# Optimization experiments

Hardware: AMD Instinct MI355X
Metric: run time of the kernel (lower is better)

The kernel has to match this reference:

```python
import jax, jax.numpy as jnp
import numpy as np

N = 65536; NPG = 4096; D_IN = 34; EMB = 34; S_DIM = 4; P_DIM = 22
WIDTH = 126; NUM_CLASSES = 8; K = 8; NUM_CONVS = 2


def setup_inputs() -> dict:
    key = jax.random.key(0)
    ks = iter(jax.random.split(key, 64))

    def w(shape, fan_in):
        return jax.random.normal(next(ks), shape, dtype=jnp.float32) / np.float32(np.sqrt(fan_in))

    inp = {
        "x": jax.random.normal(next(ks), (N, D_IN), dtype=jnp.float32),
        "conv_Ws": w((NUM_CONVS, EMB, S_DIM), EMB),
        "conv_bs": jnp.zeros((NUM_CONVS, S_DIM), jnp.float32),
        "conv_Wh": w((NUM_CONVS, EMB, P_DIM), EMB),
        "conv_bh": jnp.zeros((NUM_CONVS, P_DIM), jnp.float32),
        "conv_Wo": w((NUM_CONVS, EMB + 2 * P_DIM, EMB), EMB + 2 * P_DIM),
        "conv_bo": jnp.zeros((NUM_CONVS, EMB), jnp.float32),
    }
    for name, out_dim in (("id", NUM_CLASSES), ("reg", 4), ("chg", 1)):
        inp[name + "_W0"] = w((EMB, WIDTH), EMB)
        inp[name + "_b0"] = jnp.zeros((WIDTH,), jnp.float32)
        inp[name + "_Wh"] = w((2, WIDTH, WIDTH), WIDTH)
        inp[name + "_bh"] = jnp.zeros((2, WIDTH), jnp.float32)
        inp[name + "_Wf"] = w((WIDTH, out_dim), WIDTH)
        inp[name + "_bf"] = jnp.zeros((out_dim,), jnp.float32)
    inp["n_per_graph"] = NPG
    return inp


def _mlp(x, W0, b0, Wh, bh, Wf, bf):
    h = jax.nn.elu(x @ W0 + b0)
    h = jax.nn.elu(h @ Wh[0] + bh[0])
    h = jax.nn.elu(h @ Wh[1] + bh[1])
    return h @ Wf + bf


def _gravnet(xg, Ws, bs, Wh, bh, Wo, bo, k):
    # xg: [G, n, EMB]; equal-sized graphs (PyG batch with equal event sizes)
    s = xg @ Ws + bs  # [G, n, S_DIM] learned space coords
    h = xg @ Wh + bh  # [G, n, P_DIM] propagated features

    def per_graph(s1, h1):
        # full pairwise sq-distances in learned space (self included, d=0)
        d2 = jnp.sum((s1[:, None, :] - s1[None, :, :]) ** 2, axis=-1)  # [n, n]
        _, idx = jax.lax.top_k(-jax.lax.stop_gradient(d2), k)  # [n, k]
        s_nb = s1[idx]  # [n, k, S_DIM]
        d2k = jnp.sum((s1[:, None, :] - s_nb) ** 2, axis=-1)  # [n, k]
        w = jnp.exp(-10.0 * d2k)  # GravNet edge weight
        msg = h1[idx] * w[..., None]  # [n, k, P_DIM]
        return jnp.mean(msg, axis=1), jnp.max(msg, axis=1)

    mean_agg, max_agg = jax.vmap(per_graph)(s, h)  # [G, n, P_DIM] each
    out = jnp.concatenate([xg, mean_agg, max_agg], axis=-1) @ Wo + bo
    return out


def reference(x, conv_Ws, conv_bs, conv_Wh, conv_bh, conv_Wo, conv_bo,
              id_W0, id_b0, id_Wh, id_bh, id_Wf, id_bf,
              reg_W0, reg_b0, reg_Wh, reg_bh, reg_Wf, reg_bf,
              chg_W0, chg_b0, chg_Wh, chg_bh, chg_Wf, chg_bf,
              n_per_graph):
    n = int(n_per_graph)
    G = x.shape[0] // n
    emb = x.reshape(G, n, -1)  # native_mlpf=False: embedding = input
    for i in range(NUM_CONVS):
        emb = _gravnet(emb, conv_Ws[i], conv_bs[i], conv_Wh[i], conv_bh[i],
                       conv_Wo[i], conv_bo[i], K)
    emb = emb.reshape(x.shape[0], -1)
    preds_id = _mlp(emb, id_W0, id_b0, id_Wh, id_bh, id_Wf, id_bf)
    preds_momentum = _mlp(emb, reg_W0, reg_b0, reg_Wh, reg_bh, reg_Wf, reg_bf) + x[:, 1:5]
    pred_charge = _mlp(emb, chg_W0, chg_b0, chg_Wh, chg_bh, chg_Wf, chg_bf)
    return preds_id, preds_momentum, pred_charge
```

## Files before the change

kernel.cpp:

```cpp
#include <hip/hip_runtime.h>
#include <math.h>

#define N_NODES 65536
#define NPG     4096
#define D_IN    34
#define EMB     34
#define S_DIM   4
#define P_DIM   22
#define CONCAT  78
#define WIDTH   126
#define KNN     8
#define HPAD    24
#define EPAD    36
#define TILE    1024
#define NSPLIT  16
#define FBIG    3.4e38f
#define ASTR    133
#define WFSTR   9
#define TRUNCM  0xFFFFF000u

__device__ __forceinline__ float elu1(float v) {
    return v > 0.f ? v : expm1f(v);
}

__device__ __forceinline__ bool lexlt(float da, int ja, float db, int jb) {
    return (da < db) || (da == db && ja < jb);
}


__device__ __forceinline__ void ins4u(unsigned (&k)[4], unsigned key) {
    unsigned c = min(key, k[0]);
#pragma unroll
    for (int r = 3; r >= 1; --r) {
        const unsigned hi = max(k[r], c);
        k[r] = min(k[r], c);
        c = hi;
    }
    k[0] = c;
}

__device__ __forceinline__ void clean8u(unsigned (&k)[8]) {
#define CASU(i, j2) { const unsigned hi = max(k[i], k[j2]); \
    const unsigned lo = min(k[i], k[j2]); k[i] = hi; k[j2] = lo; }
    CASU(0,4) CASU(1,5) CASU(2,6) CASU(3,7)
    CASU(0,2) CASU(1,3) CASU(4,6) CASU(5,7)
    CASU(0,1) CASU(2,3) CASU(4,5) CASU(6,7)
#undef CASU
}

__device__ __forceinline__ void merge8u(unsigned (&k)[8], int m) {
    unsigned p[8];
#pragma unroll
    for (int i = 0; i < 8; ++i) p[i] = (unsigned)__shfl_xor((int)k[i], m);
#pragma unroll
    for (int i = 0; i < 8; ++i) k[i] = min(k[i], p[7 - i]);
    clean8u(k);
}

__device__ __forceinline__ void ins8(float (&d)[8], int (&ix)[8], float dd, int jj) {
    const bool s0 = dd < d[0];
    d[0] = s0 ? dd : d[0]; ix[0] = s0 ? jj : ix[0];
#pragma unroll
    for (int r = 0; r < 7; ++r) {
        const bool s = d[r] < d[r + 1];
        const float a = s ? d[r + 1] : d[r], b = s ? d[r] : d[r + 1];
        const int   x = s ? ix[r + 1] : ix[r], y = s ? ix[r] : ix[r + 1];
        d[r] = a; d[r + 1] = b; ix[r] = x; ix[r + 1] = y;
    }
}

__device__ __forceinline__ void clean8(float (&md)[8], int (&mj)[8]) {
#define CASL(i, k) { const bool sw = lexlt(md[i], mj[i], md[k], mj[k]); \
    const float a = sw ? md[k] : md[i], b = sw ? md[i] : md[k]; \
    const int   x = sw ? mj[k] : mj[i], y = sw ? mj[i] : mj[k]; \
    md[i] = a; md[k] = b; mj[i] = x; mj[k] = y; }
    CASL(0,4) CASL(1,5) CASL(2,6) CASL(3,7)
    CASL(0,2) CASL(1,3) CASL(4,6) CASL(5,7)
    CASL(0,1) CASL(2,3) CASL(4,5) CASL(6,7)
#undef CASL
}

__device__ __forceinline__ void merge8(float (&md)[8], int (&mj)[8], int m) {
    float pd[8]; int pj[8];
#pragma unroll
    for (int i = 0; i < 8; ++i) { pd[i] = __shfl_xor(md[i], m); pj[i] = __shfl_xor(mj[i], m); }
#pragma unroll
    for (int i = 0; i < 8; ++i) {
        const bool lt = lexlt(md[i], mj[i], pd[7 - i], pj[7 - i]);
        const float nd = lt ? md[i] : pd[7 - i];
        const int   nj = lt ? mj[i] : pj[7 - i];
        md[i] = nd; mj[i] = nj;
    }
    clean8(md, mj);
}

__global__ __launch_bounds__(256) void sh_kernel(
        const float* __restrict__ emb, int eld,
        const float* __restrict__ Ws, const float* __restrict__ bs,
        const float* __restrict__ Wh, const float* __restrict__ bh,
        float* __restrict__ s_out, float* __restrict__ h_out,
        int* __restrict__ fcnt) {
    if (blockIdx.x == 0 && threadIdx.x == 0) fcnt[0] = 0;

    __shared__ float lWs[EMB * S_DIM];
    __shared__ float lWh[EMB * P_DIM];
    __shared__ float lbs[S_DIM];
    __shared__ float lbh[P_DIM];
    for (int t = threadIdx.x; t < EMB * S_DIM; t += 256) lWs[t] = Ws[t];
    for (int t = threadIdx.x; t < EMB * P_DIM; t += 256) lWh[t] = Wh[t];
    if (threadIdx.x < S_DIM) lbs[threadIdx.x] = bs[threadIdx.x];
    if (threadIdx.x < P_DIM) lbh[threadIdx.x] = bh[threadIdx.x];
    __syncthreads();

    const int n = blockIdx.x * 256 + threadIdx.x;
    const float* __restrict__ row = emb + (size_t)n * eld;
    float e[EMB];
#pragma unroll
    for (int r = 0; r < EMB; ++r) e[r] = row[r];

    float s[S_DIM], h[P_DIM];
#pragma unroll
    for (int c = 0; c < S_DIM; ++c) s[c] = lbs[c];
#pragma unroll
    for (int c = 0; c < P_DIM; ++c) h[c] = lbh[c];
#pragma unroll
    for (int r = 0; r < EMB; ++r) {
        const float er = e[r];
#pragma unroll
        for (int c = 0; c < S_DIM; ++c) s[c] = fmaf(er, lWs[r * S_DIM + c], s[c]);
#pragma unroll
        for (int c = 0; c < P_DIM; ++c) h[c] = fmaf(er, lWh[r * P_DIM + c], h[c]);
    }
    ((float4*)s_out)[n] = make_float4(s[0], s[1], s[2], s[3]);
    float* __restrict__ hr = h_out + (size_t)n * HPAD;
#pragma unroll
    for (int c = 0; c < P_DIM; ++c) hr[c] = h[c];
}

__global__ __launch_bounds__(256, 4) void grav_scan(
        const float* __restrict__ s_buf,
        int* __restrict__ knnj,
        int* __restrict__ fcnt, int* __restrict__ flist) {
    __shared__ float4 sl[TILE];

    const int g     = blockIdx.x >> 7;
    const int chunk = blockIdx.x & 127;
    const int gbase = g * NPG;
    const int tid   = threadIdx.x;
    const int ql    = tid & 15;
    const int grp   = tid >> 4;
    const int nA    = gbase + chunk * 32 + grp * 2;
    const int nB    = nA + 1;

    const float4* __restrict__ sg = (const float4*)s_buf + gbase;
    float4 pre[4];
#pragma unroll
    for (int i = 0; i < 4; ++i) pre[i] = sg[tid + 256 * i];
    const float4 siA = ((const float4*)s_buf)[nA];
    const float4 siB = ((const float4*)s_buf)[nB];

    unsigned kA[4], kB[4];
#pragma unroll
    for (int r = 0; r < 4; ++r) { kA[r] = 0xFFFFFFFFu; kB[r] = 0xFFFFFFFFu; }

#pragma unroll
    for (int i = 0; i < 4; ++i) sl[tid + 256 * i] = pre[i];
    __syncthreads();

    for (int t = 0; t < NPG / TILE; ++t) {
        if (t < NPG / TILE - 1) {
#pragma unroll
            for (int i = 0; i < 4; ++i)
                pre[i] = sg[(t + 1) * TILE + tid + 256 * i];
        }
        unsigned suff = ((unsigned)(t << 10)) | (unsigned)ql;
#pragma unroll 4
        for (int s = 0; s < TILE / NSPLIT; ++s) {
            const float4 sj = sl[NSPLIT * s + ql];
            {
                const float dx = siA.x - sj.x, dy = siA.y - sj.y;
                const float dz = siA.z - sj.z, dw = siA.w - sj.w;
                const float d2 = fmaf(dx, dx, fmaf(dy, dy, fmaf(dz, dz, dw * dw)));
                ins4u(kA, (__float_as_uint(d2) & TRUNCM) | suff);
            }
            {
                const float dx = siB.x - sj.x, dy = siB.y - sj.y;
                const float dz = siB.z - sj.z, dw = siB.w - sj.w;
                const float d2 = fmaf(dx, dx, fmaf(dy, dy, fmaf(dz, dz, dw * dw)));
                ins4u(kB, (__float_as_uint(d2) & TRUNCM) | suff);
            }
            suff += 16u;
        }
        if (t < NPG / TILE - 1) {
            __syncthreads();
#pragma unroll
            for (int i = 0; i < 4; ++i) sl[tid + 256 * i] = pre[i];
            __syncthreads();
        }
    }

    {
        unsigned md[8];
        md[0] = kA[0]; md[1] = kA[1]; md[2] = kA[2]; md[3] = kA[3];
        md[4] = (unsigned)__shfl_xor((int)kA[3], 1);
        md[5] = (unsigned)__shfl_xor((int)kA[2], 1);
        md[6] = (unsigned)__shfl_xor((int)kA[1], 1);
        md[7] = (unsigned)__shfl_xor((int)kA[0], 1);
        clean8u(md);
        merge8u(md, 2);
        merge8u(md, 4);
        merge8u(md, 8);

        const unsigned truncW = md[0] & TRUNCM;
        int ci = 0;
#pragma unroll
        for (int r = 0; r < 4; ++r) ci += ((kA[r] & TRUNCM) <= truncW) ? 1 : 0;
        int v = ci + ((ci == 4) ? 256 : 0);
#pragma unroll
        for (int m = 1; m <= 8; m <<= 1) v += __shfl_xor(v, m);
        const bool flag = ((v & 0xFF) > 8) || ((v >> 8) != 0);

        unsigned ks = md[0];
#pragma unroll
        for (int r = 1; r < 8; ++r) { const bool p = (ql == r); ks = p ? md[r] : ks; }
        if (ql < 8)
            knnj[(size_t)nA * 8 + ql] = (int)(((ks >> 4) & 0xFFu) * 16u + (ks & 0xFu));
        if (ql == 0 && flag) {
            const int slot = atomicAdd(fcnt, 1);
            flist[slot] = nA;
        }
    }

    {
        unsigned md[8];
        md[0] = kB[0]; md[1] = kB[1]; md[2] = kB[2]; md[3] = kB[3];
        md[4] = (unsigned)__shfl_xor((int)kB[3], 1);
        md[5] = (unsigned)__shfl_xor((int)kB[2], 1);
        md[6] = (unsigned)__shfl_xor((int)kB[1], 1);
        md[7] = (unsigned)__shfl_xor((int)kB[0], 1);
        clean8u(md);
        merge8u(md, 2);
        merge8u(md, 4);
        merge8u(md, 8);

        const unsigned truncW = md[0] & TRUNCM;
        int ci = 0;
#pragma unroll
        for (int r = 0; r < 4; ++r) ci += ((kB[r] & TRUNCM) <= truncW) ? 1 : 0;
        int v = ci + ((ci == 4) ? 256 : 0);
#pragma unroll
        for (int m = 1; m <= 8; m <<= 1) v += __shfl_xor(v, m);
        const bool flag = ((v & 0xFF) > 8) || ((v >> 8) != 0);

        unsigned ks = md[0];
#pragma unroll
        for (int r = 1; r < 8; ++r) { const bool p = (ql == r); ks = p ? md[r] : ks; }
        if (ql < 8)
            knnj[(size_t)nB * 8 + ql] = (int)(((ks >> 4) & 0xFFu) * 16u + (ks & 0xFu));
        if (ql == 0 && flag) {
            const int slot = atomicAdd(fcnt, 1);
            flist[slot] = nB;
        }
    }
}

__global__ __launch_bounds__(256, 4) void grav_fix(
        const float* __restrict__ s_buf,
        int* __restrict__ knnj,
        const int* __restrict__ fcnt, const int* __restrict__ flist) {
    const int cnt = fcnt[0];
    const int ql  = threadIdx.x & 15;
    const int ngroups = gridDim.x * 16;

    for (int idx = blockIdx.x * 16 + (threadIdx.x >> 4); idx < cnt; idx += ngroups) {
        const int node = flist[idx];
        const int gbase = node & ~(NPG - 1);
        const float4 si = ((const float4*)s_buf)[node];
        const float4* __restrict__ sg = (const float4*)s_buf + gbase;

        float fd[8]; int fj[8];
#pragma unroll
        for (int r = 0; r < 8; ++r) { fd[r] = FBIG; fj[r] = 0; }
#pragma unroll 4
        for (int k = 0; k < NPG / NSPLIT; ++k) {
            const int j = NSPLIT * k + ql;
            const float4 sj = sg[j];
            const float dx = si.x - sj.x, dy = si.y - sj.y;
            const float dz = si.z - sj.z, dw = si.w - sj.w;
            const float d2 = fmaf(dx, dx, fmaf(dy, dy, fmaf(dz, dz, dw * dw)));
            ins8(fd, fj, d2, j);
        }
        merge8(fd, fj, 1);
        merge8(fd, fj, 2);
        merge8(fd, fj, 4);
        merge8(fd, fj, 8);

        int js = fj[0];
#pragma unroll
        for (int r = 1; r < 8; ++r) { const bool p = (ql == r); js = p ? fj[r] : js; }
        if (ql < 8) knnj[(size_t)node * 8 + ql] = js;
    }
}

template <int ELD, bool TOUT>
__global__ __launch_bounds__(256, 4) void grav_gather(
        const float* __restrict__ emb_in,
        const float* __restrict__ s_buf,
        const float* __restrict__ h_buf,
        const int* __restrict__ knnj,
        const float* __restrict__ Wo, const float* __restrict__ bo,
        float* __restrict__ out) {
    __shared__ float wot[EMB * 81];
    __shared__ float bol[EMB];
    __shared__ float cc[64][49];

    const int tid = threadIdx.x;
    const int q   = tid & 3;
    const int nl  = tid >> 2;
    const int node = blockIdx.x * 64 + nl;
    const int gbase = node & ~(NPG - 1);

    for (int t = tid; t < CONCAT * EMB; t += 256) {
        const int r = t / EMB, c = t % EMB;
        wot[c * 81 + r] = Wo[t];
    }
    if (tid < EMB) bol[tid] = bo[tid];

    const float4 si = ((const float4*)s_buf)[node];
    const int ja = knnj[(size_t)node * 8 + q];
    const int jb = knnj[(size_t)node * 8 + 4 + q];
    const float4 sja = ((const float4*)s_buf)[gbase + ja];
    const float4 sjb = ((const float4*)s_buf)[gbase + jb];
    float wa, wb;
    {
        const float dx = si.x - sja.x, dy = si.y - sja.y;
        const float dz = si.z - sja.z, dw = si.w - sja.w;
        wa = expf(-10.f * fmaf(dx, dx, fmaf(dy, dy, fmaf(dz, dz, dw * dw))));
    }
    {
        const float dx = si.x - sjb.x, dy = si.y - sjb.y;
        const float dz = si.z - sjb.z, dw = si.w - sjb.w;
        wb = expf(-10.f * fmaf(dx, dx, fmaf(dy, dy, fmaf(dz, dz, dw * dw))));
    }
    const float4* __restrict__ ha = (const float4*)(h_buf + (size_t)(gbase + ja) * HPAD);
    const float4* __restrict__ hb = (const float4*)(h_buf + (size_t)(gbase + jb) * HPAD);

#pragma unroll
    for (int ch = 0; ch < 6; ++ch) {
        const float4 qa = ha[ch], qb = hb[ch];
        float sx = fmaf(wa, qa.x, wb * qb.x), sy = fmaf(wa, qa.y, wb * qb.y);
        float sz = fmaf(wa, qa.z, wb * qb.z), sw = fmaf(wa, qa.w, wb * qb.w);
        float mx = fmaxf(wa * qa.x, wb * qb.x), my = fmaxf(wa * qa.y, wb * qb.y);
        float mz = fmaxf(wa * qa.z, wb * qb.z), mw = fmaxf(wa * qa.w, wb * qb.w);
#pragma unroll
        for (int m = 1; m <= 2; m <<= 1) {
            sx += __shfl_xor(sx, m); sy += __shfl_xor(sy, m);
            sz += __shfl_xor(sz, m); sw += __shfl_xor(sw, m);
            mx = fmaxf(mx, __shfl_xor(mx, m)); my = fmaxf(my, __shfl_xor(my, m));
            mz = fmaxf(mz, __shfl_xor(mz, m)); mw = fmaxf(mw, __shfl_xor(mw, m));
        }
        if (q == (ch & 3)) {
            cc[nl][ch * 4 + 0] = sx * 0.125f; cc[nl][ch * 4 + 1] = sy * 0.125f;
            cc[nl][ch * 4 + 2] = sz * 0.125f; cc[nl][ch * 4 + 3] = sw * 0.125f;
            cc[nl][24 + ch * 4 + 0] = mx; cc[nl][24 + ch * 4 + 1] = my;
            cc[nl][24 + ch * 4 + 2] = mz; cc[nl][24 + ch * 4 + 3] = mw;
        }
    }
    __syncthreads();

    float e[EMB];
    const float* __restrict__ erow = emb_in + (size_t)node * ELD;
    if constexpr (ELD == 34) {
#pragma unroll
        for (int i = 0; i < 17; ++i) {
            const float2 v = ((const float2*)erow)[i];
            e[2 * i] = v.x; e[2 * i + 1] = v.y;
        }
    } else {
#pragma unroll
        for (int i = 0; i < 8; ++i) {
            const float4 v = ((const float4*)erow)[i];
            e[4 * i] = v.x; e[4 * i + 1] = v.y; e[4 * i + 2] = v.z; e[4 * i + 3] = v.w;
        }
        const float2 v = ((const float2*)erow)[16];
        e[32] = v.x; e[33] = v.y;
    }

#pragma unroll
    for (int m = 0; m < 9; ++m) {
        const int c = q + 4 * m;
        if (c < EMB) {
            const float* __restrict__ wr = &wot[c * 81];
            float acc = bol[c];
#pragma unroll
            for (int r = 0; r < EMB; ++r)   acc = fmaf(e[r], wr[r], acc);
#pragma unroll
            for (int p = 0; p < P_DIM; ++p) acc = fmaf(cc[nl][p], wr[34 + p], acc);
#pragma unroll
            for (int p = 0; p < P_DIM; ++p) acc = fmaf(cc[nl][24 + p], wr[56 + p], acc);
            if constexpr (TOUT)
                out[(size_t)c * N_NODES + node] = acc;
            else
                out[(size_t)node * EPAD + c] = acc;
        }
    }
}

__global__ __launch_bounds__(512, 4) void heads_fused(
        const float* __restrict__ emb2T,
        const float* __restrict__ xin,
        float* __restrict__ outp,
        const float* __restrict__ W0a, const float* __restrict__ b0a,
        const float* __restrict__ Wha, const float* __restrict__ bha,
        const float* __restrict__ Wfa, const float* __restrict__ bfa,
        const float* __restrict__ W0b, const float* __restrict__ b0b,
        const float* __restrict__ Whb, const float* __restrict__ bhb,
        const float* __restrict__ Wfb, const float* __restrict__ bfb,
        const float* __restrict__ W0c, const float* __restrict__ b0c,
        const float* __restrict__ Whc, const float* __restrict__ bhc,
        const float* __restrict__ Wfc, const float* __restrict__ bfc) {
    __shared__ float sA[WIDTH * ASTR];
    __shared__ float sWf[128 * WFSTR];

    const int tid  = threadIdx.x;
    const int head = blockIdx.x % 3;
    const int rowbase = (blockIdx.x / 3) * 128;
    const int lane = tid & 63;
    const int wave = __builtin_amdgcn_readfirstlane(tid >> 6);
    int colbase = wave * 16;
    if (colbase > WIDTH - 16) colbase = WIDTH - 16;

    const float* W0 = head == 0 ? W0a : head == 1 ? W0b : W0c;
    const float* b0 = head == 0 ? b0a : head == 1 ? b0b : b0c;
    const float* Wh = head == 0 ? Wha : head == 1 ? Whb : Whc;
    const float* bh = head == 0 ? bha : head == 1 ? bhb : bhc;
    const float* Wf = head == 0 ? Wfa : head == 1 ? Wfb : Wfc;
    const float* bf = head == 0 ? bfa : head == 1 ? bfb : bfc;
    const int odim  = head == 0 ? 8 : head == 1 ? 4 : 1;
    const size_t ooff = head == 0 ? 0
                      : head == 1 ? (size_t)N_NODES * 8 : (size_t)N_NODES * 12;

    for (int t = tid; t < 128 * 8; t += 512) {
        const int k = t >> 3, o = t & 7;
        sWf[k * WFSTR + o] = (k < WIDTH && o < odim) ? Wf[k * odim + o] : 0.f;
    }

    float accA[16], accB[16];

#pragma unroll
    for (int o = 0; o < 16; ++o) { accA[o] = b0[colbase + o]; accB[o] = accA[o]; }
#pragma unroll 2
    for (int k = 0; k < EMB; ++k) {
        const float xa = emb2T[(size_t)k * N_NODES + rowbase + lane];
        const float xb = emb2T[(size_t)k * N_NODES + rowbase + lane + 64];
        const float* __restrict__ wr = W0 + (size_t)k * WIDTH + colbase;
#pragma unroll
        for (int o = 0; o < 16; ++o) {
            const float w = wr[o];
            accA[o] = fmaf(xa, w, accA[o]);
            accB[o] = fmaf(xb, w, accB[o]);
        }
    }
    __syncthreads();
#pragma unroll
    for (int o = 0; o < 16; ++o) {
        sA[(colbase + o) * ASTR + lane]      = elu1(accA[o]);
        sA[(colbase + o) * ASTR + lane + 64] = elu1(accB[o]);
    }
    __syncthreads();

#pragma unroll
    for (int o = 0; o < 16; ++o) { accA[o] = bh[colbase + o]; accB[o] = accA[o]; }
#pragma unroll 2
    for (int k = 0; k < WIDTH; ++k) {
        const float xa = sA[k * ASTR + lane];
        const float xb = sA[k * ASTR + lane + 64];
        const float* __restrict__ wr = Wh + (size_t)k * WIDTH + colbase;
#pragma unroll
        for (int o = 0; o < 16; ++o) {
            const float w = wr[o];
            accA[o] = fmaf(xa, w, accA[o]);
            accB[o] = fmaf(xb, w, accB[o]);
        }
    }
    __syncthreads();
#pragma unroll
    for (int o = 0; o < 16; ++o) {
        sA[(colbase + o) * ASTR + lane]      = elu1(accA[o]);
        sA[(colbase + o) * ASTR + lane + 64] = elu1(accB[o]);
    }
    __syncthreads();

#pragma unroll
    for (int o = 0; o < 16; ++o) { accA[o] = bh[WIDTH + colbase + o]; accB[o] = accA[o]; }
#pragma unroll 2
    for (int k = 0; k < WIDTH; ++k) {
        const float xa = sA[k * ASTR + lane];
        const float xb = sA[k * ASTR + lane + 64];
        const float* __restrict__ wr = Wh + (size_t)(WIDTH + k) * WIDTH + colbase;
#pragma unroll
        for (int o = 0; o < 16; ++o) {
            const float w = wr[o];
            accA[o] = fmaf(xa, w, accA[o]);
            accB[o] = fmaf(xb, w, accB[o]);
        }
    }
    __syncthreads();
#pragma unroll
    for (int o = 0; o < 16; ++o) {
        sA[(colbase + o) * ASTR + lane]      = elu1(accA[o]);
        sA[(colbase + o) * ASTR + lane + 64] = elu1(accB[o]);
    }
    __syncthreads();

#pragma unroll 2
    for (int r = 0; r < 16; ++r) {
        const int rowl = wave * 16 + r;
        const float xa0 = sA[lane * ASTR + rowl];
        const float xa1 = (lane + 64 < WIDTH) ? sA[(lane + 64) * ASTR + rowl] : 0.f;
        float pa[8];
#pragma unroll
        for (int o = 0; o < 8; ++o) {
            const float w0 = sWf[lane * WFSTR + o];
            const float w1 = sWf[(lane + 64) * WFSTR + o];
            pa[o] = fmaf(xa0, w0, xa1 * w1);
        }
#pragma unroll
        for (int m = 1; m <= 32; m <<= 1) {
#pragma unroll
            for (int o = 0; o < 8; ++o) pa[o] += __shfl_xor(pa[o], m);
        }
        if (lane < odim) {
            float v = pa[0];
#pragma unroll
            for (int o = 1; o < 8; ++o) { const bool p = (lane == o); v = p ? pa[o] : v; }
            v += bf[lane];
            const int grow = rowbase + rowl;
            if (head == 1) v += xin[(size_t)grow * D_IN + 1 + lane];
            outp[ooff + (size_t)grow * odim + lane] = v;
        }
    }
}

extern "C" void kernel_launch(void* const* d_in, const int* in_sizes, int n_in,
                              void* d_out, int out_size, void* d_ws, size_t ws_size,
                              hipStream_t stream) {
    (void)in_sizes; (void)n_in; (void)out_size;

    const float* x   = (const float*)d_in[0];
    const float* cWs = (const float*)d_in[1];
    const float* cbs = (const float*)d_in[2];
    const float* cWh = (const float*)d_in[3];
    const float* cbh = (const float*)d_in[4];
    const float* cWo = (const float*)d_in[5];
    const float* cbo = (const float*)d_in[6];
    const float* hW0[3] = {(const float*)d_in[7],  (const float*)d_in[13], (const float*)d_in[19]};
    const float* hb0[3] = {(const float*)d_in[8],  (const float*)d_in[14], (const float*)d_in[20]};
    const float* hWh[3] = {(const float*)d_in[9],  (const float*)d_in[15], (const float*)d_in[21]};
    const float* hbh[3] = {(const float*)d_in[10], (const float*)d_in[16], (const float*)d_in[22]};
    const float* hWf[3] = {(const float*)d_in[11], (const float*)d_in[17], (const float*)d_in[23]};
    const float* hbf[3] = {(const float*)d_in[12], (const float*)d_in[18], (const float*)d_in[24]};
    float* outp = (float*)d_out;
    float* ws = (float*)d_ws;

    const size_t OFF_S   = 0;
    const size_t OFF_H   = OFF_S   + (size_t)N_NODES * 4;
    const size_t OFF_E1  = OFF_H   + (size_t)N_NODES * HPAD;
    const size_t OFF_E2T = OFF_E1  + (size_t)N_NODES * EPAD;
    const size_t OFF_KS  = OFF_E2T + (size_t)EMB * N_NODES;
    const size_t WS_END  = OFF_KS  + (size_t)N_NODES * 10;
    if (ws_size < WS_END * sizeof(float)) return;

    float* s_buf  = ws + OFF_S;
    float* h_buf  = ws + OFF_H;
    float* emb1   = ws + OFF_E1;
    float* emb2T  = ws + OFF_E2T;
    int*   knnj   = (int*)(ws + OFF_KS);
    int*   flist  = (int*)(ws + OFF_KS + (size_t)N_NODES * 8);
    int*   fcnt   = (int*)(ws + OFF_KS + (size_t)N_NODES * 9);

    sh_kernel<<<256, 256, 0, stream>>>(x, D_IN, cWs, cbs, cWh, cbh, s_buf, h_buf, fcnt);
    grav_scan<<<2048, 256, 0, stream>>>(s_buf, knnj, fcnt, flist);
    grav_fix<<<256, 256, 0, stream>>>(s_buf, knnj, fcnt, flist);
    grav_gather<34, false><<<1024, 256, 0, stream>>>(x, s_buf, h_buf, knnj, cWo, cbo, emb1);

    sh_kernel<<<256, 256, 0, stream>>>(emb1, EPAD, cWs + EMB * S_DIM, cbs + S_DIM,
                                       cWh + EMB * P_DIM, cbh + P_DIM, s_buf, h_buf, fcnt);
    grav_scan<<<2048, 256, 0, stream>>>(s_buf, knnj, fcnt, flist);
    grav_fix<<<256, 256, 0, stream>>>(s_buf, knnj, fcnt, flist);
    grav_gather<36, true><<<1024, 256, 0, stream>>>(emb1, s_buf, h_buf, knnj,
                                                    cWo + CONCAT * EMB, cbo + EMB, emb2T);

    heads_fused<<<1536, 512, 0, stream>>>(
        emb2T, x, outp,
        hW0[0], hb0[0], hWh[0], hbh[0], hWf[0], hbf[0],
        hW0[1], hb0[1], hWh[1], hbh[1], hWf[1], hbf[1],
        hW0[2], hb0[2], hWh[2], hbh[2], hWf[2], hbf[2]);
}
```

Before: 776.0 us.

## Run MLP heads on bf16 MFMA with split hi/lo precision emulation

Replaces the scalar-FMA MLP heads kernel with one that uses 16x16x32 bf16 MFMA instructions. Activations and weights are each split into bf16 hi and lo parts, and three MFMAs per tile recover close to fp32 accuracy. A new prep kernel packs the head weights into the fragment layout each call. Each block now handles 64 rows, with activations kept in LDS as bf16 hi/lo. The aim is to move the dominant GEMM work from vector ALUs onto matrix cores, at the cost of three times the MFMA count and a small amount of precision loss.

```diff
diff --git a/kernel.cpp b/kernel.cpp
--- a/kernel.cpp
+++ b/kernel.cpp
@@ -15,9 +15,14 @@
 #define TILE    1024
 #define NSPLIT  16
 #define FBIG    3.4e38f
-#define ASTR    133
-#define WFSTR   9
 #define TRUNCM  0xFFFFF000u
+
+#define KSTR    136
+#define WSEG0   0
+#define WSEG1   8192
+#define WSEG2   24576
+#define WSEG3   40960
+#define WHEAD   43008
 
 __device__ __forceinline__ float elu1(float v) {
     return v > 0.f ? v : expm1f(v);
@@ -27,6 +32,13 @@
     return (da < db) || (da == db && ja < jb);
 }
 
+__device__ __forceinline__ unsigned short f2bf(float v) {
+    const unsigned u = __float_as_uint(v);
+    return (unsigned short)((u + 0x7FFFu + ((u >> 16) & 1u)) >> 16);
+}
+__device__ __forceinline__ float bf2f(unsigned short h) {
+    return __uint_as_float(((unsigned)h) << 16);
+}
 
 __device__ __forceinline__ void ins4u(unsigned (&k)[4], unsigned key) {
     unsigned c = min(key, k[0]);
@@ -406,138 +418,185 @@
     }
 }
 
-__global__ __launch_bounds__(512, 4) void heads_fused(
+__global__ __launch_bounds__(256) void prep_wfrag(
+        const float* __restrict__ W0a, const float* __restrict__ Wha, const float* __restrict__ Wfa,
+        const float* __restrict__ W0b, const float* __restrict__ Whb, const float* __restrict__ Wfb,
+        const float* __restrict__ W0c, const float* __restrict__ Whc, const float* __restrict__ Wfc,
+        unsigned short* __restrict__ whi, unsigned short* __restrict__ wlo) {
+    const int head = blockIdx.y;
+    const int e = blockIdx.x * 256 + threadIdx.x;
+
+    const float* W0 = head == 0 ? W0a : head == 1 ? W0b : W0c;
+    const float* Wh = head == 0 ? Wha : head == 1 ? Whb : Whc;
+    const float* Wf = head == 0 ? Wfa : head == 1 ? Wfb : Wfc;
+    const int odim  = head == 0 ? 8 : head == 1 ? 4 : 1;
+
+    int k, n, K, N, NT, ld, segbase;
+    const float* src;
+    if (e < WSEG1) {
+        const int e2 = e;      k = e2 >> 7; n = e2 & 127;
+        K = EMB; N = WIDTH; NT = 8; ld = WIDTH; src = W0; segbase = WSEG0;
+    } else if (e < WSEG2) {
+        const int e2 = e - WSEG1; k = e2 >> 7; n = e2 & 127;
+        K = WIDTH; N = WIDTH; NT = 8; ld = WIDTH; src = Wh; segbase = WSEG1;
+    } else if (e < WSEG3) {
+        const int e2 = e - WSEG2; k = e2 >> 7; n = e2 & 127;
+        K = WIDTH; N = WIDTH; NT = 8; ld = WIDTH; src = Wh + WIDTH * WIDTH; segbase = WSEG2;
+    } else {
+        const int e2 = e - WSEG3; k = e2 >> 4; n = e2 & 15;
+        K = WIDTH; N = odim; NT = 1; ld = odim; src = Wf; segbase = WSEG3;
+    }
+
+    const float val = (k < K && n < N) ? src[k * ld + n] : 0.f;
+    const unsigned short h = f2bf(val);
+    const unsigned short l = f2bf(val - bf2f(h));
+
+    const int ks = k >> 5, ko = k & 31, nt = n >> 4;
+    const int pos = (((ks * NT + nt) * 64) + ((ko >> 3) * 16) + (n & 15)) * 8 + (ko & 7);
+    whi[(size_t)head * WHEAD + segbase + pos] = h;
+    wlo[(size_t)head * WHEAD + segbase + pos] = l;
+}
+
+typedef __attribute__((ext_vector_type(8))) short bf8;
+typedef __attribute__((ext_vector_type(4))) float f32x4;
+
+__global__ __launch_bounds__(256, 3) void heads_mfma(
         const float* __restrict__ emb2T,
         const float* __restrict__ xin,
         float* __restrict__ outp,
-        const float* __restrict__ W0a, const float* __restrict__ b0a,
-        const float* __restrict__ Wha, const float* __restrict__ bha,
-        const float* __restrict__ Wfa, const float* __restrict__ bfa,
-        const float* __restrict__ W0b, const float* __restrict__ b0b,
-        const float* __restrict__ Whb, const float* __restrict__ bhb,
-        const float* __restrict__ Wfb, const float* __restrict__ bfb,
-        const float* __restrict__ W0c, const float* __restrict__ b0c,
-        const float* __restrict__ Whc, const float* __restrict__ bhc,
-        const float* __restrict__ Wfc, const float* __restrict__ bfc) {
-    __shared__ float sA[WIDTH * ASTR];
-    __shared__ float sWf[128 * WFSTR];
+        const unsigned short* __restrict__ whi,
+        const unsigned short* __restrict__ wlo,
+        const float* __restrict__ b0a, const float* __restrict__ bha, const float* __restrict__ bfa,
+        const float* __restrict__ b0b, const float* __restrict__ bhb, const float* __restrict__ bfb,
+        const float* __restrict__ b0c, const float* __restrict__ bhc, const float* __restrict__ bfc) {
+    __shared__ unsigned short aH[64 * KSTR];
+    __shared__ unsigned short aL[64 * KSTR];
+    __shared__ float pf[4 * 64 * 16];
 
     const int tid  = threadIdx.x;
     const int head = blockIdx.x % 3;
-    const int rowbase = (blockIdx.x / 3) * 128;
-    const int lane = tid & 63;
-    const int wave = __builtin_amdgcn_readfirstlane(tid >> 6);
-    int colbase = wave * 16;
-    if (colbase > WIDTH - 16) colbase = WIDTH - 16;
-
-    const float* W0 = head == 0 ? W0a : head == 1 ? W0b : W0c;
+    const int rowbase = (blockIdx.x / 3) * 64;
+    const int w = tid >> 6;
+    const int l = tid & 63;
+
+    const unsigned short* WH = whi + (size_t)head * WHEAD;
+    const unsigned short* WL = wlo + (size_t)head * WHEAD;
     const float* b0 = head == 0 ? b0a : head == 1 ? b0b : b0c;
-    const float* Wh = head == 0 ? Wha : head == 1 ? Whb : Whc;
     const float* bh = head == 0 ? bha : head == 1 ? bhb : bhc;
-    const float* Wf = head == 0 ? Wfa : head == 1 ? Wfb : Wfc;
     const float* bf = head == 0 ? bfa : head == 1 ? bfb : bfc;
     const int odim  = head == 0 ? 8 : head == 1 ? 4 : 1;
     const size_t ooff = head == 0 ? 0
                       : head == 1 ? (size_t)N_NODES * 8 : (size_t)N_NODES * 12;
 
-    for (int t = tid; t < 128 * 8; t += 512) {
-        const int k = t >> 3, o = t & 7;
-        sWf[k * WFSTR + o] = (k < WIDTH && o < odim) ? Wf[k * odim + o] : 0.f;
-    }
-
-    float accA[16], accB[16];
-
-#pragma unroll
-    for (int o = 0; o < 16; ++o) { accA[o] = b0[colbase + o]; accB[o] = accA[o]; }
-#pragma unroll 2
-    for (int k = 0; k < EMB; ++k) {
-        const float xa = emb2T[(size_t)k * N_NODES + rowbase + lane];
-        const float xb = emb2T[(size_t)k * N_NODES + rowbase + lane + 64];
-        const float* __restrict__ wr = W0 + (size_t)k * WIDTH + colbase;
-#pragma unroll
-        for (int o = 0; o < 16; ++o) {
-            const float w = wr[o];
-            accA[o] = fmaf(xa, w, accA[o]);
-            accB[o] = fmaf(xb, w, accB[o]);
-        }
+    for (int t = tid; t < 64 * 64; t += 256) {
+        const int r = t & 63, k = t >> 6;
+        const float v = (k < EMB) ? emb2T[(size_t)k * N_NODES + rowbase + r] : 0.f;
+        const unsigned short h = f2bf(v);
+        aH[r * KSTR + k] = h;
+        aL[r * KSTR + k] = f2bf(v - bf2f(h));
     }
     __syncthreads();
-#pragma unroll
-    for (int o = 0; o < 16; ++o) {
-        sA[(colbase + o) * ASTR + lane]      = elu1(accA[o]);
-        sA[(colbase + o) * ASTR + lane + 64] = elu1(accB[o]);
-    }
-    __syncthreads();
-
-#pragma unroll
-    for (int o = 0; o < 16; ++o) { accA[o] = bh[colbase + o]; accB[o] = accA[o]; }
-#pragma unroll 2
-    for (int k = 0; k < WIDTH; ++k) {
-        const float xa = sA[k * ASTR + lane];
-        const float xb = sA[k * ASTR + lane + 64];
-        const float* __restrict__ wr = Wh + (size_t)k * WIDTH + colbase;
-#pragma unroll
-        for (int o = 0; o < 16; ++o) {
-            const float w = wr[o];
-            accA[o] = fmaf(xa, w, accA[o]);
-            accB[o] = fmaf(xb, w, accB[o]);
-        }
-    }
-    __syncthreads();
-#pragma unroll
-    for (int o = 0; o < 16; ++o) {
-        sA[(colbase + o) * ASTR + lane]      = elu1(accA[o]);
-        sA[(colbase + o) * ASTR + lane + 64] = elu1(accB[o]);
-    }
-    __syncthreads();
-
-#pragma unroll
-    for (int o = 0; o < 16; ++o) { accA[o] = bh[WIDTH + colbase + o]; accB[o] = accA[o]; }
-#pragma unroll 2
-    for (int k = 0; k < WIDTH; ++k) {
-        const float xa = sA[k * ASTR + lane];
-        const float xb = sA[k * ASTR + lane + 64];
-        const float* __restrict__ wr = Wh + (size_t)(WIDTH + k) * WIDTH + colbase;
-#pragma unroll
-        for (int o = 0; o < 16; ++o) {
-            const float w = wr[o];
-            accA[o] = fmaf(xa, w, accA[o]);
-            accB[o] = fmaf(xb, w, accB[o]);
-        }
-    }
-    __syncthreads();
-#pragma unroll
-    for (int o = 0; o < 16; ++o) {
-        sA[(colbase + o) * ASTR + lane]      = elu1(accA[o]);
-        sA[(colbase + o) * ASTR + lane + 64] = elu1(accB[o]);
-    }
-    __syncthreads();
-
-#pragma unroll 2
-    for (int r = 0; r < 16; ++r) {
-        const int rowl = wave * 16 + r;
-        const float xa0 = sA[lane * ASTR + rowl];
-        const float xa1 = (lane + 64 < WIDTH) ? sA[(lane + 64) * ASTR + rowl] : 0.f;
-        float pa[8];
-#pragma unroll
-        for (int o = 0; o < 8; ++o) {
-            const float w0 = sWf[lane * WFSTR + o];
-            const float w1 = sWf[(lane + 64) * WFSTR + o];
-            pa[o] = fmaf(xa0, w0, xa1 * w1);
-        }
-#pragma unroll
-        for (int m = 1; m <= 32; m <<= 1) {
-#pragma unroll
-            for (int o = 0; o < 8; ++o) pa[o] += __shfl_xor(pa[o], m);
-        }
-        if (lane < odim) {
-            float v = pa[0];
-#pragma unroll
-            for (int o = 1; o < 8; ++o) { const bool p = (lane == o); v = p ? pa[o] : v; }
-            v += bf[lane];
-            const int grow = rowbase + rowl;
-            if (head == 1) v += xin[(size_t)grow * D_IN + 1 + lane];
-            outp[ooff + (size_t)grow * odim + lane] = v;
+
+    const int lm = l & 15;
+    const int lk = (l >> 4) * 8;
+
+#pragma unroll
+    for (int layer = 0; layer < 3; ++layer) {
+        const int KS = (layer == 0) ? 2 : 4;
+        const int seg = (layer == 0) ? WSEG0 : (layer == 1) ? WSEG1 : WSEG2;
+        const float* bias = (layer == 0) ? b0 : (layer == 1) ? bh : bh + WIDTH;
+
+        f32x4 acc[4][2];
+#pragma unroll
+        for (int nt2 = 0; nt2 < 2; ++nt2) {
+            const int col = (w * 2 + nt2) * 16 + lm;
+            const float bv = (col < WIDTH) ? bias[col] : 0.f;
+#pragma unroll
+            for (int mt = 0; mt < 4; ++mt)
+                acc[mt][nt2] = f32x4{bv, bv, bv, bv};
+        }
+
+        for (int ks = 0; ks < KS; ++ks) {
+            bf8 bh0, bh1, bl0, bl1;
+            {
+                const size_t o0 = ((size_t)(ks * 8 + w * 2 + 0) * 64 + l) * 8;
+                const size_t o1 = ((size_t)(ks * 8 + w * 2 + 1) * 64 + l) * 8;
+                bh0 = *(const bf8*)(WH + seg + o0);
+                bh1 = *(const bf8*)(WH + seg + o1);
+                bl0 = *(const bf8*)(WL + seg + o0);
+                bl1 = *(const bf8*)(WL + seg + o1);
+            }
+#pragma unroll
+            for (int mt = 0; mt < 4; ++mt) {
+                const int aoff = (mt * 16 + lm) * KSTR + ks * 32 + lk;
+                const bf8 ah = *(const bf8*)&aH[aoff];
+                const bf8 al = *(const bf8*)&aL[aoff];
+                acc[mt][0] = __builtin_amdgcn_mfma_f32_16x16x32_bf16(ah, bh0, acc[mt][0], 0, 0, 0);
+                acc[mt][0] = __builtin_amdgcn_mfma_f32_16x16x32_bf16(ah, bl0, acc[mt][0], 0, 0, 0);
+                acc[mt][0] = __builtin_amdgcn_mfma_f32_16x16x32_bf16(al, bh0, acc[mt][0], 0, 0, 0);
+                acc[mt][1] = __builtin_amdgcn_mfma_f32_16x16x32_bf16(ah, bh1, acc[mt][1], 0, 0, 0);
+                acc[mt][1] = __builtin_amdgcn_mfma_f32_16x16x32_bf16(ah, bl1, acc[mt][1], 0, 0, 0);
+                acc[mt][1] = __builtin_amdgcn_mfma_f32_16x16x32_bf16(al, bh1, acc[mt][1], 0, 0, 0);
+            }
+        }
+        __syncthreads();
+
+#pragma unroll
+        for (int mt = 0; mt < 4; ++mt) {
+#pragma unroll
+            for (int nt2 = 0; nt2 < 2; ++nt2) {
+                const int col = (w * 2 + nt2) * 16 + lm;
+#pragma unroll
+                for (int r = 0; r < 4; ++r) {
+                    const int row = mt * 16 + (l >> 4) * 4 + r;
+                    const float v = elu1(acc[mt][nt2][r]);
+                    const unsigned short h = f2bf(v);
+                    aH[row * KSTR + col] = h;
+                    aL[row * KSTR + col] = f2bf(v - bf2f(h));
+                }
+            }
+        }
+        __syncthreads();
+    }
+
+    {
+        f32x4 facc[4];
+#pragma unroll
+        for (int mt = 0; mt < 4; ++mt) facc[mt] = f32x4{0.f, 0.f, 0.f, 0.f};
+
+        const int ks = w;
+        const size_t o0 = ((size_t)(ks * 1 + 0) * 64 + l) * 8;
+        const bf8 bh0 = *(const bf8*)(WH + WSEG3 + o0);
+        const bf8 bl0 = *(const bf8*)(WL + WSEG3 + o0);
+#pragma unroll
+        for (int mt = 0; mt < 4; ++mt) {
+            const int aoff = (mt * 16 + lm) * KSTR + ks * 32 + lk;
+            const bf8 ah = *(const bf8*)&aH[aoff];
+            const bf8 al = *(const bf8*)&aL[aoff];
+            facc[mt] = __builtin_amdgcn_mfma_f32_16x16x32_bf16(ah, bh0, facc[mt], 0, 0, 0);
+            facc[mt] = __builtin_amdgcn_mfma_f32_16x16x32_bf16(ah, bl0, facc[mt], 0, 0, 0);
+            facc[mt] = __builtin_amdgcn_mfma_f32_16x16x32_bf16(al, bh0, facc[mt], 0, 0, 0);
+        }
+#pragma unroll
+        for (int mt = 0; mt < 4; ++mt) {
+#pragma unroll
+            for (int r = 0; r < 4; ++r) {
+                const int row = mt * 16 + (l >> 4) * 4 + r;
+                pf[(w * 64 + row) * 16 + lm] = facc[mt][r];
+            }
+        }
+        __syncthreads();
+
+        const int sh = head == 0 ? 3 : head == 1 ? 2 : 0;
+        for (int e = tid; e < 64 * odim; e += 256) {
+            const int row = e >> sh;
+            const int o = e & (odim - 1);
+            float v = pf[(0 * 64 + row) * 16 + o] + pf[(1 * 64 + row) * 16 + o]
+                    + pf[(2 * 64 + row) * 16 + o] + pf[(3 * 64 + row) * 16 + o];
+            v += bf[o];
+            const int grow = rowbase + row;
+            if (head == 1) v += xin[(size_t)grow * D_IN + 1 + o];
+            outp[ooff + (size_t)grow * odim + o] = v;
         }
     }
 }
@@ -568,7 +627,9 @@
     const size_t OFF_E1  = OFF_H   + (size_t)N_NODES * HPAD;
     const size_t OFF_E2T = OFF_E1  + (size_t)N_NODES * EPAD;
     const size_t OFF_KS  = OFF_E2T + (size_t)EMB * N_NODES;
-    const size_t WS_END  = OFF_KS  + (size_t)N_NODES * 10;
+    const size_t OFF_WH  = OFF_KS  + (size_t)N_NODES * 10;
+    const size_t OFF_WL  = OFF_WH  + (3 * WHEAD + 1) / 2;
+    const size_t WS_END  = OFF_WL  + (3 * WHEAD + 1) / 2;
     if (ws_size < WS_END * sizeof(float)) return;
 
     float* s_buf  = ws + OFF_S;
@@ -578,6 +639,12 @@
     int*   knnj   = (int*)(ws + OFF_KS);
     int*   flist  = (int*)(ws + OFF_KS + (size_t)N_NODES * 8);
     int*   fcnt   = (int*)(ws + OFF_KS + (size_t)N_NODES * 9);
+    unsigned short* whi = (unsigned short*)(ws + OFF_WH);
+    unsigned short* wlo = (unsigned short*)(ws + OFF_WL);
+
+    prep_wfrag<<<dim3(168, 3), 256, 0, stream>>>(
+        hW0[0], hWh[0], hWf[0], hW0[1], hWh[1], hWf[1], hW0[2], hWh[2], hWf[2],
+        whi, wlo);
 
     sh_kernel<<<256, 256, 0, stream>>>(x, D_IN, cWs, cbs, cWh, cbh, s_buf, h_buf, fcnt);
     grav_scan<<<2048, 256, 0, stream>>>(s_buf, knnj, fcnt, flist);
@@ -591,9 +658,9 @@
     grav_gather<36, true><<<1024, 256, 0, stream>>>(emb1, s_buf, h_buf, knnj,
                                                     cWo + CONCAT * EMB, cbo + EMB, emb2T);
 
-    heads_fused<<<1536, 512, 0, stream>>>(
-        emb2T, x, outp,
-        hW0[0], hb0[0], hWh[0], hbh[0], hWf[0], hbf[0],
-        hW0[1], hb0[1], hWh[1], hbh[1], hWf[1], hbf[1],
-        hW0[2], hb0[2], hWh[2], hbh[2], hWf[2], hbf[2]);
-}
+    heads_mfma<<<3072, 256, 0, stream>>>(
+        emb2T, x, outp, whi, wlo,
+        hb0[0], hbh[0], hbf[0],
+        hb0[1], hbh[1], hbf[1],
+        hb0[2], hbh[2], hbf[2]);
+}
```

New measurement: 645.2 us. 1.2x faster.
